# Optimization experiments

Hardware: AMD Instinct MI355X
Metric: run time of the kernel (lower is better)

The kernel has to match this reference:

```python
import jax, jax.numpy as jnp
import numpy as np

B, T, C, H = 2, 2048, 2048, 16
HD = C // H  # 128 head dim
ROPE_BASE = 10000.0


def setup_inputs() -> dict:
    key = jax.random.key(0)
    k0, k1, k2 = jax.random.split(key, 3)
    x = jax.random.normal(k0, (B, T, C), dtype=jnp.float32)
    W_attn = jax.random.normal(k1, (C, 3 * C), dtype=jnp.float32) * 0.02
    b_attn = jnp.zeros((3 * C,), dtype=jnp.float32)
    W_proj = jax.random.normal(k2, (C, C), dtype=jnp.float32) * 0.02
    b_proj = jnp.zeros((C,), dtype=jnp.float32)
    # freqs_cis = exp(i * t * theta_j), represented as (cos, sin), shape [T, HD//2]
    inv_freq = 1.0 / (ROPE_BASE ** (jnp.arange(0, HD, 2, dtype=jnp.float32) / HD))
    freqs = jnp.outer(jnp.arange(T, dtype=jnp.float32), inv_freq)
    return {"x": x, "W_attn": W_attn, "b_attn": b_attn, "W_proj": W_proj,
            "b_proj": b_proj, "cos": jnp.cos(freqs), "sin": jnp.sin(freqs)}


def _apply_rope(v, cos, sin):
    # v: [B, T, H, HD]; pairs (v[..., 2i], v[..., 2i+1]) rotated by angle freqs[t, i]
    vr = v.reshape(v.shape[:-1] + (-1, 2))
    x0, x1 = vr[..., 0], vr[..., 1]
    c = cos[None, :, None, :]  # [1, T, 1, HD//2]
    s = sin[None, :, None, :]
    o0 = x0 * c - x1 * s
    o1 = x0 * s + x1 * c
    return jnp.stack([o0, o1], axis=-1).reshape(v.shape)


def reference(x, W_attn, b_attn, W_proj, b_proj, cos, sin):
    Bv, Tv, Cv = x.shape
    qkv = x @ W_attn + b_attn                      # [B, T, 3C]
    q, k, v = jnp.split(qkv, 3, axis=-1)
    q = q.reshape(Bv, Tv, H, HD)
    k = k.reshape(Bv, Tv, H, HD)
    v = v.reshape(Bv, Tv, H, HD)
    q = _apply_rope(q, cos, sin)
    k = _apply_rope(k, cos, sin)
    scale = 1.0 / jnp.sqrt(jnp.float32(HD))
    att = jnp.einsum('bqhd,bkhd->bhqk', q, k) * scale
    causal = jnp.tril(jnp.ones((Tv, Tv), dtype=bool))
    att = jnp.where(causal[None, None], att, jnp.finfo(att.dtype).min)
    att = jax.nn.softmax(att, axis=-1)
    y = jnp.einsum('bhqk,bkhd->bqhd', att, v).reshape(Bv, Tv, Cv)
    return y @ W_proj + b_proj
```

## Files before the change

kernel.cpp:

```cpp
#include <hip/hip_runtime.h>

typedef unsigned short u16;
typedef __attribute__((ext_vector_type(8))) short short8;
typedef __attribute__((ext_vector_type(4))) float f32x4;

#define TSEQ 2048
#define NHEAD 16
#define HDIM 128

__device__ __forceinline__ u16 f2bf(float x) {
    unsigned u = __float_as_uint(x);
    return (u16)((u + 0x7fffu + ((u >> 16) & 1u)) >> 16);
}
__device__ __forceinline__ float b2f(u16 h) {
    return __uint_as_float(((unsigned)h) << 16);
}
__device__ __forceinline__ void async16(const void* g, void* l) {
    __builtin_amdgcn_global_load_lds((__attribute__((address_space(1))) void*)(void*)g,
                                     (__attribute__((address_space(3))) void*)l, 16, 0, 0);
}
__device__ __forceinline__ f32x4 zero4() {
    f32x4 z = {0.f, 0.f, 0.f, 0.f};
    return z;
}

template <int CTRL>
__device__ __forceinline__ float dppf(float x) {
    return __int_as_float(__builtin_amdgcn_mov_dpp(__float_as_int(x), CTRL, 0xf, 0xf, true));
}
__device__ __forceinline__ float dpp_max16(float x) {
    x = fmaxf(x, dppf<0xB1>(x));
    x = fmaxf(x, dppf<0x4E>(x));
    x = fmaxf(x, dppf<0x141>(x));
    x = fmaxf(x, dppf<0x140>(x));
    return x;
}
__device__ __forceinline__ float dpp_sum16(float x) {
    x += dppf<0xB1>(x);
    x += dppf<0x4E>(x);
    x += dppf<0x141>(x);
    x += dppf<0x140>(x);
    return x;
}

__global__ void cast_bf16(const float4* __restrict__ in, ushort4* __restrict__ out, int n4) {
    int i = blockIdx.x * 256 + threadIdx.x;
    if (i < n4) {
        float4 v = in[i];
        ushort4 o;
        o.x = f2bf(v.x); o.y = f2bf(v.y); o.z = f2bf(v.z); o.w = f2bf(v.w);
        out[i] = o;
    }
}

__global__ void transpose_cast(const float* __restrict__ in, u16* __restrict__ out, int K, int N) {
    __shared__ float tile[64][65];
    int n0 = blockIdx.x * 64, k0 = blockIdx.y * 64;
    int tx = threadIdx.x & 63, ty = threadIdx.x >> 6;
#pragma unroll
    for (int i = 0; i < 16; i++) {
        int r = ty + i * 4;
        tile[r][tx] = in[(size_t)(k0 + r) * N + n0 + tx];
    }
    __syncthreads();
#pragma unroll
    for (int i = 0; i < 16; i++) {
        int r = ty + i * 4;
        out[(size_t)(n0 + r) * K + k0 + tx] = f2bf(tile[tx][r]);
    }
}

template <int MODE>
__global__ __launch_bounds__(256) void gemm_bt(
    const u16* __restrict__ A, const u16* __restrict__ Bt, const float* __restrict__ bias,
    float* __restrict__ outf, u16* __restrict__ qb, u16* __restrict__ kb, u16* __restrict__ vT,
    const float* __restrict__ cosp, const float* __restrict__ sinp,
    int M, int N, int K) {
    __shared__ __align__(16) u16 smem[8704];
    u16* As = smem;
    u16* Bs = smem + 4096;
    const int tid = threadIdx.x;
    const int wave = tid >> 6, lane = tid & 63;
    const int low = lane & 15, quad = lane >> 4;
    const int m0 = blockIdx.y * 128, n0 = blockIdx.x * 128;
    const int wm = (wave >> 1) * 64, wn = (wave & 1) * 64;
    const int ldr = lane >> 2;
    const int ldc = (lane & 3) * 8;

    f32x4 acc[4][4];
#pragma unroll
    for (int i = 0; i < 4; i++)
#pragma unroll
        for (int j = 0; j < 4; j++) acc[i][j] = zero4();

    for (int k0 = 0; k0 < K; k0 += 32) {
#pragma unroll
        for (int c = 0; c < 2; ++c) {
            const int chunk = wave * 2 + c;
            const int row = chunk * 16 + ldr;
            async16(A + (size_t)(m0 + row) * K + k0 + ldc, As + chunk * 512);
            async16(Bt + (size_t)(n0 + row) * K + k0 + ldc, Bs + chunk * 512);
        }
        __syncthreads();
        short8 af[4], bfv[4];
#pragma unroll
        for (int i = 0; i < 4; i++) af[i] = *(const short8*)(As + (wm + i * 16 + low) * 32 + quad * 8);
#pragma unroll
        for (int j = 0; j < 4; j++) bfv[j] = *(const short8*)(Bs + (wn + j * 16 + low) * 32 + quad * 8);
#pragma unroll
        for (int i = 0; i < 4; i++)
#pragma unroll
            for (int j = 0; j < 4; j++)
                acc[i][j] = __builtin_amdgcn_mfma_f32_16x16x32_bf16(af[i], bfv[j], acc[i][j], 0, 0, 0);
        __syncthreads();
    }

    if (MODE == 1) {
#pragma unroll
        for (int j = 0; j < 4; j++) {
            const int ng = n0 + wn + j * 16 + low;
            const float bv = bias[ng];
#pragma unroll
            for (int i = 0; i < 4; i++) {
                const int rbase = m0 + wm + i * 16 + quad * 4;
#pragma unroll
                for (int r = 0; r < 4; r++)
                    outf[(size_t)(rbase + r) * N + ng] = acc[i][j][r] + bv;
            }
        }
        return;
    }

    const int which = n0 >> 11;
    const int h = (n0 & 2047) >> 7;
    const int b = m0 >> 11, t0 = m0 & 2047;
    float bv[4];
#pragma unroll
    for (int j = 0; j < 4; j++) bv[j] = bias[n0 + wn + j * 16 + low];
    u16* epi = smem;

    if (which < 2) {
        u16* dst = (which == 0 ? qb : kb) + (((size_t)(b * NHEAD + h)) * TSEQ + t0) * HDIM;
#pragma unroll
        for (int pass = 0; pass < 2; pass++) {
            if ((wave >> 1) == pass) {
#pragma unroll
                for (int i = 0; i < 4; i++)
#pragma unroll
                    for (int j = 0; j < 4; j++)
#pragma unroll
                        for (int r = 0; r < 4; r++)
                            epi[(i * 16 + quad * 4 + r) * 136 + wn + j * 16 + low] =
                                f2bf(acc[i][j][r] + bv[j]);
            }
            __syncthreads();
            const int row = tid >> 2, dq = tid & 3;
            const int t = t0 + pass * 64 + row;
            const float* cb = cosp + (size_t)t * 64 + dq * 16;
            const float* sb = sinp + (size_t)t * 64 + dq * 16;
            const u16* er = epi + row * 136 + dq * 32;
            u16* dr = dst + (size_t)(pass * 64 + row) * HDIM + dq * 32;
#pragma unroll
            for (int half = 0; half < 2; half++) {
                u16 vals[16];
                *(short8*)(vals) = *(const short8*)(er + half * 16);
                *(short8*)(vals + 8) = *(const short8*)(er + half * 16 + 8);
                float cs[8], sn[8];
                *(float4*)(cs) = *(const float4*)(cb + half * 8);
                *(float4*)(cs + 4) = *(const float4*)(cb + half * 8 + 4);
                *(float4*)(sn) = *(const float4*)(sb + half * 8);
                *(float4*)(sn + 4) = *(const float4*)(sb + half * 8 + 4);
                u16 ov[16];
#pragma unroll
                for (int p = 0; p < 8; p++) {
                    float x0 = b2f(vals[2 * p]), x1 = b2f(vals[2 * p + 1]);
                    ov[2 * p] = f2bf(x0 * cs[p] - x1 * sn[p]);
                    ov[2 * p + 1] = f2bf(x0 * sn[p] + x1 * cs[p]);
                }
                *(short8*)(dr + half * 16) = *(const short8*)(ov);
                *(short8*)(dr + half * 16 + 8) = *(const short8*)(ov + 8);
            }
            __syncthreads();
        }
    } else {
        u16* dst = vT + ((size_t)(b * NHEAD + h)) * HDIM * TSEQ + t0;
#pragma unroll
        for (int pass = 0; pass < 2; pass++) {
            if ((wave & 1) == pass) {
#pragma unroll
                for (int i = 0; i < 4; i++)
#pragma unroll
                    for (int j = 0; j < 4; j++)
#pragma unroll
                        for (int r = 0; r < 4; r++)
                            epi[(j * 16 + low) * 136 + wm + i * 16 + quad * 4 + r] =
                                f2bf(acc[i][j][r] + bv[j]);
            }
            __syncthreads();
            const int drow = tid >> 2, tc = (tid & 3) * 32;
            u16* dr = dst + (size_t)(pass * 64 + drow) * TSEQ + tc;
#pragma unroll
            for (int q = 0; q < 4; q++)
                *(short8*)(dr + q * 8) = *(const short8*)(epi + drow * 136 + tc + q * 8);
            __syncthreads();
        }
    }
}

__global__ __launch_bounds__(256, 2) void flash_attn(const u16* __restrict__ qg, const u16* __restrict__ kg,
                                                     const u16* __restrict__ vT, u16* __restrict__ y) {
    __shared__ u16 Ks[2][64 * 128];
    __shared__ u16 Vs[2][128 * 64];
    __shared__ u16 Ps[4][16 * 72];
    const int tid = threadIdx.x;
    const int wave = tid >> 6, lane = tid & 63;
    const int low = lane & 15, quad = lane >> 4;
    const int bh = blockIdx.x;
    const int qt = 15 - blockIdx.y;
    const int qa = qt * 128 + wave * 16;
    const int qbr = qa + 64;
    const float scale2 = 0.08838834764831845f * 1.44269504088896f;

    const u16* Qp = qg + (size_t)bh * TSEQ * HDIM;
    short8 qfA[4], qfB[4];
#pragma unroll
    for (int c = 0; c < 4; c++) {
        qfA[c] = *(const short8*)(Qp + (size_t)(qa + low) * HDIM + c * 32 + quad * 8);
        qfB[c] = *(const short8*)(Qp + (size_t)(qbr + low) * HDIM + c * 32 + quad * 8);
    }

    f32x4 oA[8], oB[8];
#pragma unroll
    for (int d = 0; d < 8; d++) { oA[d] = zero4(); oB[d] = zero4(); }
    float mA[4], lA[4], mB[4], lB[4];
#pragma unroll
    for (int r = 0; r < 4; r++) { mA[r] = -1e30f; lA[r] = 0.f; mB[r] = -1e30f; lB[r] = 0.f; }

    const u16* Kb = kg + (size_t)bh * TSEQ * HDIM;
    const u16* Vb = vT + (size_t)bh * HDIM * TSEQ;
    u16* Pw = &Ps[wave][0];
    const int ntiles = 2 * qt + 2;

    const int krow = tid >> 4, kchunk = tid & 15;
    const int vrow = tid >> 3, vchunk = tid & 7;

#pragma unroll
    for (int j = 0; j < 4; j++) {
        const int row = j * 16 + krow;
        async16(Kb + (size_t)row * HDIM + (kchunk ^ (row & 7)) * 8, Ks[0] + row * 128 + kchunk * 8);
    }
#pragma unroll
    for (int j = 0; j < 4; j++) {
        const int d = j * 32 + vrow;
        async16(Vb + (size_t)d * TSEQ + (vchunk ^ (d & 7)) * 8, Vs[0] + d * 64 + vchunk * 8);
    }

    for (int kt = 0; kt < ntiles; ++kt) {
        const int kv0 = kt * 64;
        const int cur = kt & 1;
        __syncthreads();

        if (kt + 1 < ntiles) {
            const int nkv = kv0 + 64;
            u16* kd = Ks[cur ^ 1];
            u16* vd = Vs[cur ^ 1];
#pragma unroll
            for (int j = 0; j < 4; j++) {
                const int row = j * 16 + krow;
                async16(Kb + (size_t)(nkv + row) * HDIM + (kchunk ^ (row & 7)) * 8,
                        kd + row * 128 + kchunk * 8);
            }
#pragma unroll
            for (int j = 0; j < 4; j++) {
                const int d = j * 32 + vrow;
                async16(Vb + (size_t)d * TSEQ + nkv + (vchunk ^ (d & 7)) * 8, vd + d * 64 + vchunk * 8);
            }
        }

        const u16* Kc = Ks[cur];
        const u16* Vc = Vs[cur];
        const bool activeA = (kv0 <= qa + 15);

        f32x4 sA[4], sB[4];
#pragma unroll
        for (int h = 0; h < 4; h++) { sA[h] = zero4(); sB[h] = zero4(); }
#pragma unroll
        for (int h = 0; h < 4; h++) {
            const int row = h * 16 + low;
#pragma unroll
            for (int c = 0; c < 4; c++) {
                short8 kf = *(const short8*)(Kc + row * 128 + (((c * 4 + quad) ^ (row & 7))) * 8);
                sA[h] = __builtin_amdgcn_mfma_f32_16x16x32_bf16(qfA[c], kf, sA[h], 0, 0, 0);
                sB[h] = __builtin_amdgcn_mfma_f32_16x16x32_bf16(qfB[c], kf, sB[h], 0, 0, 0);
            }
        }

        short8 pfA[2], pfB[2];
        float alA[4], alB[4];
        if (activeA) {
#pragma unroll
            for (int r = 0; r < 4; r++) {
                const int qrow = qa + quad * 4 + r;
                float sv[4];
#pragma unroll
                for (int h = 0; h < 4; h++)
                    sv[h] = (kv0 + h * 16 + low <= qrow) ? sA[h][r] * scale2 : -1e30f;
                float mx = fmaxf(fmaxf(sv[0], sv[1]), fmaxf(sv[2], sv[3]));
                mx = dpp_max16(mx);
                float mnew = fmaxf(mA[r], mx);
                alA[r] = exp2f(mA[r] - mnew);
                mA[r] = mnew;
                float p0 = exp2f(sv[0] - mnew), p1 = exp2f(sv[1] - mnew);
                float p2 = exp2f(sv[2] - mnew), p3 = exp2f(sv[3] - mnew);
                float rs = (p0 + p1) + (p2 + p3);
                rs = dpp_sum16(rs);
                lA[r] = lA[r] * alA[r] + rs;
                const int prow = (quad * 4 + r) * 72;
                Pw[prow + low] = f2bf(p0);
                Pw[prow + 16 + low] = f2bf(p1);
                Pw[prow + 32 + low] = f2bf(p2);
                Pw[prow + 48 + low] = f2bf(p3);
            }
            __threadfence_block();
#pragma unroll
            for (int kc = 0; kc < 2; kc++)
                pfA[kc] = *(const short8*)(Pw + low * 72 + kc * 32 + quad * 8);
        }
        {
#pragma unroll
            for (int r = 0; r < 4; r++) {
                const int qrow = qbr + quad * 4 + r;
                float sv[4];
#pragma unroll
                for (int h = 0; h < 4; h++)
                    sv[h] = (kv0 + h * 16 + low <= qrow) ? sB[h][r] * scale2 : -1e30f;
                float mx = fmaxf(fmaxf(sv[0], sv[1]), fmaxf(sv[2], sv[3]));
                mx = dpp_max16(mx);
                float mnew = fmaxf(mB[r], mx);
                alB[r] = exp2f(mB[r] - mnew);
                mB[r] = mnew;
                float p0 = exp2f(sv[0] - mnew), p1 = exp2f(sv[1] - mnew);
                float p2 = exp2f(sv[2] - mnew), p3 = exp2f(sv[3] - mnew);
                float rs = (p0 + p1) + (p2 + p3);
                rs = dpp_sum16(rs);
                lB[r] = lB[r] * alB[r] + rs;
                const int prow = (quad * 4 + r) * 72;
                Pw[prow + low] = f2bf(p0);
                Pw[prow + 16 + low] = f2bf(p1);
                Pw[prow + 32 + low] = f2bf(p2);
                Pw[prow + 48 + low] = f2bf(p3);
            }
            __threadfence_block();
#pragma unroll
            for (int kc = 0; kc < 2; kc++)
                pfB[kc] = *(const short8*)(Pw + low * 72 + kc * 32 + quad * 8);
        }

        if (activeA) {
#pragma unroll
            for (int d = 0; d < 8; ++d)
#pragma unroll
                for (int r = 0; r < 4; r++) { oA[d][r] *= alA[r]; oB[d][r] *= alB[r]; }
#pragma unroll
            for (int kc = 0; kc < 2; kc++)
#pragma unroll
                for (int dd = 0; dd < 8; ++dd) {
                    const int vr = dd * 16 + low;
                    short8 vf = *(const short8*)(Vc + vr * 64 + (((kc * 4 + quad) ^ (vr & 7))) * 8);
                    oA[dd] = __builtin_amdgcn_mfma_f32_16x16x32_bf16(pfA[kc], vf, oA[dd], 0, 0, 0);
                    oB[dd] = __builtin_amdgcn_mfma_f32_16x16x32_bf16(pfB[kc], vf, oB[dd], 0, 0, 0);
                }
        } else {
#pragma unroll
            for (int d = 0; d < 8; ++d)
#pragma unroll
                for (int r = 0; r < 4; r++) oB[d][r] *= alB[r];
#pragma unroll
            for (int kc = 0; kc < 2; kc++)
#pragma unroll
                for (int dd = 0; dd < 8; ++dd) {
                    const int vr = dd * 16 + low;
                    short8 vf = *(const short8*)(Vc + vr * 64 + (((kc * 4 + quad) ^ (vr & 7))) * 8);
                    oB[dd] = __builtin_amdgcn_mfma_f32_16x16x32_bf16(pfB[kc], vf, oB[dd], 0, 0, 0);
                }
        }
    }

    const int b = bh >> 4, h = bh & 15;
#pragma unroll
    for (int r = 0; r < 4; r++) {
        float invA = 1.0f / lA[r];
        float invB = 1.0f / lB[r];
        size_t rowA = (size_t)(b * TSEQ + qa + quad * 4 + r);
        size_t rowB = (size_t)(b * TSEQ + qbr + quad * 4 + r);
        u16* ypA = y + rowA * 2048 + h * HDIM;
        u16* ypB = y + rowB * 2048 + h * HDIM;
#pragma unroll
        for (int d = 0; d < 8; ++d) {
            ypA[d * 16 + low] = f2bf(oA[d][r] * invA);
            ypB[d * 16 + low] = f2bf(oB[d][r] * invB);
        }
    }
}

extern "C" void kernel_launch(void* const* d_in, const int* in_sizes, int n_in,
                              void* d_out, int out_size, void* d_ws, size_t ws_size,
                              hipStream_t stream) {
    const float* x = (const float*)d_in[0];
    const float* Wa = (const float*)d_in[1];
    const float* ba = (const float*)d_in[2];
    const float* Wp = (const float*)d_in[3];
    const float* bp = (const float*)d_in[4];
    const float* cs = (const float*)d_in[5];
    const float* sn = (const float*)d_in[6];
    float* out = (float*)d_out;

    u16* xb = (u16*)d_ws;
    u16* Wab = xb + 8388608;
    u16* Wpb = Wab + 12582912;
    u16* qb = Wpb + 4194304;
    u16* kb = qb + 8388608;
    u16* vT = kb + 8388608;
    u16* y = xb;

    cast_bf16<<<8192, 256, 0, stream>>>((const float4*)x, (ushort4*)xb, 2097152);
    transpose_cast<<<dim3(96, 32), 256, 0, stream>>>(Wa, Wab, 2048, 6144);
    transpose_cast<<<dim3(32, 32), 256, 0, stream>>>(Wp, Wpb, 2048, 2048);
    gemm_bt<0><<<dim3(48, 32), 256, 0, stream>>>(xb, Wab, ba, nullptr, qb, kb, vT, cs, sn, 4096, 6144, 2048);
    flash_attn<<<dim3(32, 16), 256, 0, stream>>>(qb, kb, vT, y);
    gemm_bt<1><<<dim3(16, 32), 256, 0, stream>>>(y, Wpb, bp, out, nullptr, nullptr, nullptr, nullptr, nullptr, 4096, 2048, 2048);
}
```

Measured before the change: 468.9 us.

## Unfuse RoPE from QKV GEMM epilogue into separate in-place kernel

```diff
diff --git a/kernel.cpp b/kernel.cpp
--- a/kernel.cpp
+++ b/kernel.cpp
@@ -7,6 +7,7 @@
 #define TSEQ 2048
 #define NHEAD 16
 #define HDIM 128
+#define NQKV 6144
 
 __device__ __forceinline__ u16 f2bf(float x) {
     unsigned u = __float_as_uint(x);
@@ -73,8 +74,7 @@
 template <int MODE>
 __global__ __launch_bounds__(256) void gemm_bt(
     const u16* __restrict__ A, const u16* __restrict__ Bt, const float* __restrict__ bias,
-    float* __restrict__ outf, u16* __restrict__ qb, u16* __restrict__ kb, u16* __restrict__ vT,
-    const float* __restrict__ cosp, const float* __restrict__ sinp,
+    float* __restrict__ outf, u16* __restrict__ qkvb, u16* __restrict__ vT,
     int M, int N, int K) {
     __shared__ __align__(16) u16 smem[8704];
     u16* As = smem;
@@ -131,58 +131,26 @@
         return;
     }
 
-    const int which = n0 >> 11;
-    const int h = (n0 & 2047) >> 7;
-    const int b = m0 >> 11, t0 = m0 & 2047;
-    float bv[4];
-#pragma unroll
-    for (int j = 0; j < 4; j++) bv[j] = bias[n0 + wn + j * 16 + low];
-    u16* epi = smem;
-
-    if (which < 2) {
-        u16* dst = (which == 0 ? qb : kb) + (((size_t)(b * NHEAD + h)) * TSEQ + t0) * HDIM;
-#pragma unroll
-        for (int pass = 0; pass < 2; pass++) {
-            if ((wave >> 1) == pass) {
-#pragma unroll
-                for (int i = 0; i < 4; i++)
-#pragma unroll
-                    for (int j = 0; j < 4; j++)
-#pragma unroll
-                        for (int r = 0; r < 4; r++)
-                            epi[(i * 16 + quad * 4 + r) * 136 + wn + j * 16 + low] =
-                                f2bf(acc[i][j][r] + bv[j]);
-            }
-            __syncthreads();
-            const int row = tid >> 2, dq = tid & 3;
-            const int t = t0 + pass * 64 + row;
-            const float* cb = cosp + (size_t)t * 64 + dq * 16;
-            const float* sb = sinp + (size_t)t * 64 + dq * 16;
-            const u16* er = epi + row * 136 + dq * 32;
-            u16* dr = dst + (size_t)(pass * 64 + row) * HDIM + dq * 32;
-#pragma unroll
-            for (int half = 0; half < 2; half++) {
-                u16 vals[16];
-                *(short8*)(vals) = *(const short8*)(er + half * 16);
-                *(short8*)(vals + 8) = *(const short8*)(er + half * 16 + 8);
-                float cs[8], sn[8];
-                *(float4*)(cs) = *(const float4*)(cb + half * 8);
-                *(float4*)(cs + 4) = *(const float4*)(cb + half * 8 + 4);
-                *(float4*)(sn) = *(const float4*)(sb + half * 8);
-                *(float4*)(sn + 4) = *(const float4*)(sb + half * 8 + 4);
-                u16 ov[16];
-#pragma unroll
-                for (int p = 0; p < 8; p++) {
-                    float x0 = b2f(vals[2 * p]), x1 = b2f(vals[2 * p + 1]);
-                    ov[2 * p] = f2bf(x0 * cs[p] - x1 * sn[p]);
-                    ov[2 * p + 1] = f2bf(x0 * sn[p] + x1 * cs[p]);
-                }
-                *(short8*)(dr + half * 16) = *(const short8*)(ov);
-                *(short8*)(dr + half * 16 + 8) = *(const short8*)(ov + 8);
-            }
-            __syncthreads();
+    if (n0 < 4096) {
+#pragma unroll
+        for (int j = 0; j < 4; j++) {
+            const int ng = n0 + wn + j * 16 + low;
+            const float bv = bias[ng];
+#pragma unroll
+            for (int i = 0; i < 4; i++) {
+                const int rbase = m0 + wm + i * 16 + quad * 4;
+#pragma unroll
+                for (int r = 0; r < 4; r++)
+                    qkvb[(size_t)(rbase + r) * NQKV + ng] = f2bf(acc[i][j][r] + bv);
+            }
         }
     } else {
+        const int h = (n0 & 2047) >> 7;
+        const int b = m0 >> 11, t0 = m0 & 2047;
+        float bv[4];
+#pragma unroll
+        for (int j = 0; j < 4; j++) bv[j] = bias[n0 + wn + j * 16 + low];
+        u16* epi = smem;
         u16* dst = vT + ((size_t)(b * NHEAD + h)) * HDIM * TSEQ + t0;
 #pragma unroll
         for (int pass = 0; pass < 2; pass++) {
@@ -207,7 +175,25 @@
     }
 }
 
-__global__ __launch_bounds__(256, 2) void flash_attn(const u16* __restrict__ qg, const u16* __restrict__ kg,
+__global__ void rope_inplace(u16* __restrict__ qkvb, const float* __restrict__ cosp,
+                             const float* __restrict__ sinp) {
+    int idx = blockIdx.x * 256 + threadIdx.x;
+    int p = idx & 1023;
+    int row = idx >> 10;
+    int t = row & (TSEQ - 1);
+    int i = p & 63;
+    size_t o = (size_t)row * NQKV + (p >> 6) * HDIM + 2 * i;
+    float c = cosp[t * 64 + i], s = sinp[t * 64 + i];
+    float q0 = b2f(qkvb[o]), q1 = b2f(qkvb[o + 1]);
+    qkvb[o] = f2bf(q0 * c - q1 * s);
+    qkvb[o + 1] = f2bf(q0 * s + q1 * c);
+    size_t ok = o + 2048;
+    float k0 = b2f(qkvb[ok]), k1 = b2f(qkvb[ok + 1]);
+    qkvb[ok] = f2bf(k0 * c - k1 * s);
+    qkvb[ok + 1] = f2bf(k0 * s + k1 * c);
+}
+
+__global__ __launch_bounds__(256, 2) void flash_attn(const u16* __restrict__ qkvb,
                                                      const u16* __restrict__ vT, u16* __restrict__ y) {
     __shared__ u16 Ks[2][64 * 128];
     __shared__ u16 Vs[2][128 * 64];
@@ -217,16 +203,18 @@
     const int low = lane & 15, quad = lane >> 4;
     const int bh = blockIdx.x;
     const int qt = 15 - blockIdx.y;
+    const int b = bh >> 4, h = bh & 15;
     const int qa = qt * 128 + wave * 16;
     const int qbr = qa + 64;
     const float scale2 = 0.08838834764831845f * 1.44269504088896f;
 
-    const u16* Qp = qg + (size_t)bh * TSEQ * HDIM;
+    const u16* Qb = qkvb + (size_t)(b * TSEQ) * NQKV + h * HDIM;
+    const u16* Kb = qkvb + (size_t)(b * TSEQ) * NQKV + 2048 + h * HDIM;
     short8 qfA[4], qfB[4];
 #pragma unroll
     for (int c = 0; c < 4; c++) {
-        qfA[c] = *(const short8*)(Qp + (size_t)(qa + low) * HDIM + c * 32 + quad * 8);
-        qfB[c] = *(const short8*)(Qp + (size_t)(qbr + low) * HDIM + c * 32 + quad * 8);
+        qfA[c] = *(const short8*)(Qb + (size_t)(qa + low) * NQKV + c * 32 + quad * 8);
+        qfB[c] = *(const short8*)(Qb + (size_t)(qbr + low) * NQKV + c * 32 + quad * 8);
     }
 
     f32x4 oA[8], oB[8];
@@ -236,7 +224,6 @@
 #pragma unroll
     for (int r = 0; r < 4; r++) { mA[r] = -1e30f; lA[r] = 0.f; mB[r] = -1e30f; lB[r] = 0.f; }
 
-    const u16* Kb = kg + (size_t)bh * TSEQ * HDIM;
     const u16* Vb = vT + (size_t)bh * HDIM * TSEQ;
     u16* Pw = &Ps[wave][0];
     const int ntiles = 2 * qt + 2;
@@ -247,7 +234,7 @@
 #pragma unroll
     for (int j = 0; j < 4; j++) {
         const int row = j * 16 + krow;
-        async16(Kb + (size_t)row * HDIM + (kchunk ^ (row & 7)) * 8, Ks[0] + row * 128 + kchunk * 8);
+        async16(Kb + (size_t)row * NQKV + (kchunk ^ (row & 7)) * 8, Ks[0] + row * 128 + kchunk * 8);
     }
 #pragma unroll
     for (int j = 0; j < 4; j++) {
@@ -267,7 +254,7 @@
 #pragma unroll
             for (int j = 0; j < 4; j++) {
                 const int row = j * 16 + krow;
-                async16(Kb + (size_t)(nkv + row) * HDIM + (kchunk ^ (row & 7)) * 8,
+                async16(Kb + (size_t)(nkv + row) * NQKV + (kchunk ^ (row & 7)) * 8,
                         kd + row * 128 + kchunk * 8);
             }
 #pragma unroll
@@ -283,15 +270,15 @@
 
         f32x4 sA[4], sB[4];
 #pragma unroll
-        for (int h = 0; h < 4; h++) { sA[h] = zero4(); sB[h] = zero4(); }
-#pragma unroll
-        for (int h = 0; h < 4; h++) {
-            const int row = h * 16 + low;
+        for (int h2 = 0; h2 < 4; h2++) { sA[h2] = zero4(); sB[h2] = zero4(); }
+#pragma unroll
+        for (int h2 = 0; h2 < 4; h2++) {
+            const int row = h2 * 16 + low;
 #pragma unroll
             for (int c = 0; c < 4; c++) {
                 short8 kf = *(const short8*)(Kc + row * 128 + (((c * 4 + quad) ^ (row & 7))) * 8);
-                sA[h] = __builtin_amdgcn_mfma_f32_16x16x32_bf16(qfA[c], kf, sA[h], 0, 0, 0);
-                sB[h] = __builtin_amdgcn_mfma_f32_16x16x32_bf16(qfB[c], kf, sB[h], 0, 0, 0);
+                sA[h2] = __builtin_amdgcn_mfma_f32_16x16x32_bf16(qfA[c], kf, sA[h2], 0, 0, 0);
+                sB[h2] = __builtin_amdgcn_mfma_f32_16x16x32_bf16(qfB[c], kf, sB[h2], 0, 0, 0);
             }
         }
 
@@ -303,8 +290,8 @@
                 const int qrow = qa + quad * 4 + r;
                 float sv[4];
 #pragma unroll
-                for (int h = 0; h < 4; h++)
-                    sv[h] = (kv0 + h * 16 + low <= qrow) ? sA[h][r] * scale2 : -1e30f;
+                for (int h2 = 0; h2 < 4; h2++)
+                    sv[h2] = (kv0 + h2 * 16 + low <= qrow) ? sA[h2][r] * scale2 : -1e30f;
                 float mx = fmaxf(fmaxf(sv[0], sv[1]), fmaxf(sv[2], sv[3]));
                 mx = dpp_max16(mx);
                 float mnew = fmaxf(mA[r], mx);
@@ -332,8 +319,8 @@
                 const int qrow = qbr + quad * 4 + r;
                 float sv[4];
 #pragma unroll
-                for (int h = 0; h < 4; h++)
-                    sv[h] = (kv0 + h * 16 + low <= qrow) ? sB[h][r] * scale2 : -1e30f;
+                for (int h2 = 0; h2 < 4; h2++)
+                    sv[h2] = (kv0 + h2 * 16 + low <= qrow) ? sB[h2][r] * scale2 : -1e30f;
                 float mx = fmaxf(fmaxf(sv[0], sv[1]), fmaxf(sv[2], sv[3]));
                 mx = dpp_max16(mx);
                 float mnew = fmaxf(mB[r], mx);
@@ -386,7 +373,6 @@
         }
     }
 
-    const int b = bh >> 4, h = bh & 15;
 #pragma unroll
     for (int r = 0; r < 4; r++) {
         float invA = 1.0f / lA[r];
@@ -418,15 +404,15 @@
     u16* xb = (u16*)d_ws;
     u16* Wab = xb + 8388608;
     u16* Wpb = Wab + 12582912;
-    u16* qb = Wpb + 4194304;
-    u16* kb = qb + 8388608;
-    u16* vT = kb + 8388608;
+    u16* qkvb = Wpb + 4194304;
+    u16* vT = qkvb + 25165824;
     u16* y = xb;
 
     cast_bf16<<<8192, 256, 0, stream>>>((const float4*)x, (ushort4*)xb, 2097152);
     transpose_cast<<<dim3(96, 32), 256, 0, stream>>>(Wa, Wab, 2048, 6144);
     transpose_cast<<<dim3(32, 32), 256, 0, stream>>>(Wp, Wpb, 2048, 2048);
-    gemm_bt<0><<<dim3(48, 32), 256, 0, stream>>>(xb, Wab, ba, nullptr, qb, kb, vT, cs, sn, 4096, 6144, 2048);
-    flash_attn<<<dim3(32, 16), 256, 0, stream>>>(qb, kb, vT, y);
-    gemm_bt<1><<<dim3(16, 32), 256, 0, stream>>>(y, Wpb, bp, out, nullptr, nullptr, nullptr, nullptr, nullptr, 4096, 2048, 2048);
-}
+    gemm_bt<0><<<dim3(48, 32), 256, 0, stream>>>(xb, Wab, ba, nullptr, qkvb, vT, 4096, 6144, 2048);
+    rope_inplace<<<16384, 256, 0, stream>>>(qkvb, cs, sn);
+    flash_attn<<<dim3(32, 16), 256, 0, stream>>>(qkvb, vT, y);
+    gemm_bt<1><<<dim3(16, 32), 256, 0, stream>>>(y, Wpb, bp, out, nullptr, nullptr, 4096, 2048, 2048);
+}
```

Measured after the change: 472.0 us. No clear change (+0.7%).
